# Kernel optimization log

Hardware: AMD Instinct MI355X
Metric: run time of the kernel (lower is better)

## Reference

```python
import jax, jax.numpy as jnp
import numpy as np
import math

L, B = 1024, 256
SEQ_DIM, KMER_DIM, HID = 16, 256, 64
N_LAYERS = 2
IN_DIM = SEQ_DIM + KMER_DIM + 21  # 293


def _normalize(v, eps=1e-12):
    return v / jnp.maximum(jnp.linalg.norm(v, axis=-1, keepdims=True), eps)


def _nerf_rot(a, b, c):
    # rotation matrix with columns [bc, n x bc, n] from last three backbone points
    bc = _normalize(c - b)
    n = _normalize(jnp.cross(b - a, bc))
    return jnp.stack([bc, jnp.cross(n, bc), n], axis=-1)  # (..., 3, 3)


def pnerf(c_tilde, nfrag):
    # c_tilde: (3L, B, 3) SRF coordinates; parallelized natural extension of reference frame
    Ltot, batch = c_tilde.shape[0], c_tilde.shape[1]
    k = Ltot // nfrag
    # contiguous fragments of length k, folded into the batch dim: (k, nfrag*B, 3)
    x = c_tilde.reshape(nfrag, k, batch, 3).transpose(1, 0, 2, 3).reshape(k, nfrag * batch, 3)
    init = jnp.array([[-math.sqrt(0.5), math.sqrt(1.5), 0.0],
                      [-math.sqrt(2.0), 0.0, 0.0],
                      [0.0, 0.0, 0.0]], dtype=c_tilde.dtype)
    F = nfrag * batch
    carry0 = (jnp.broadcast_to(init[0], (F, 3)),
              jnp.broadcast_to(init[1], (F, 3)),
              jnp.broadcast_to(init[2], (F, 3)))

    def extend(carry, ct):
        a, b, c = carry
        R = _nerf_rot(a, b, c)                      # (F, 3, 3)
        d = c + jnp.einsum('fij,fj->fi', R, ct)     # (F, 3)
        return (b, c, d), d

    _, frag = jax.lax.scan(extend, carry0, x)        # (k, F, 3)
    frag = frag.reshape(k, nfrag, batch, 3).transpose(1, 0, 2, 3)  # (nfrag, k, B, 3)

    # assemble fragments sequentially; init frame is identity/origin so frag 0 passes through
    carryA = (jnp.broadcast_to(init[0], (batch, 3)),
              jnp.broadcast_to(init[1], (batch, 3)),
              jnp.broadcast_to(init[2], (batch, 3)))

    def assemble(carry, fr):
        a, b, c = carry
        R = _nerf_rot(a, b, c)                      # (B, 3, 3)
        y = c + jnp.einsum('bij,kbj->kbi', R, fr)   # (k, B, 3)
        return (y[-3], y[-2], y[-1]), y

    _, ys = jax.lax.scan(assemble, carryA, frag)     # (nfrag, k, B, 3)
    return ys.reshape(nfrag * k, batch, 3)


def setup_inputs() -> dict:
    key = jax.random.key(0)
    ks = jax.random.split(key, 12)
    s = 0.05
    return {
        'seq': jax.random.randint(ks[0], (L, B), 0, 20, dtype=jnp.int64),
        'kmer': jax.random.randint(ks[1], (L, B), 0, 22 ** 3, dtype=jnp.int64),
        'pssm': jax.random.uniform(ks[2], (L, B, 21), dtype=jnp.float32),
        'length': jax.random.randint(ks[3], (L,), 1, L, dtype=jnp.int64),
        'seq_embed': jax.random.normal(ks[4], (20, SEQ_DIM), dtype=jnp.float32) * s,
        'kmer_embed': jax.random.normal(ks[5], (22 ** 3, KMER_DIM), dtype=jnp.float32) * s,
        'W0': jax.random.normal(ks[6], (IN_DIM, HID), dtype=jnp.float32) * s,
        'b0': jnp.zeros((HID,), dtype=jnp.float32),
        'We': jax.random.normal(ks[7], (HID, HID), dtype=jnp.float32) * s,
        'be': jnp.zeros((HID,), dtype=jnp.float32),
        'W1': jax.random.normal(ks[8], (HID, 9), dtype=jnp.float32) * s,
        'b1': jnp.zeros((9,), dtype=jnp.float32),
    }


def reference(seq, kmer, pssm, length, seq_embed, kmer_embed, W0, b0, We, be, W1, b1):
    s = seq_embed[seq]                                   # (L, B, 16)
    km = kmer_embed[kmer]                                # (L, B, 256)
    h = jnp.concatenate([s, km, pssm], axis=2)           # (L, B, 293)
    h = h @ W0 + b0                                      # (L, B, 64)
    # torch list-multiplication shares the SAME Linear across the n_layers blocks
    for _ in range(N_LAYERS):
        h = jax.nn.relu(h @ We + be)                     # dropout is identity at eval
    srf = h @ W1 + b1                                    # (L, B, 9)
    Ld, Bd = srf.shape[0], srf.shape[1]
    srf = srf.reshape(Ld, Bd, 3, 3).transpose(0, 2, 1, 3).reshape(3 * Ld, Bd, 3)
    return pnerf(srf, int(math.sqrt(Ld)))
```

## Files before the change

### kernel.cpp

```cpp
#include <hip/hip_runtime.h>
#include <math.h>

#define HPAD 72

typedef short bf16x8 __attribute__((ext_vector_type(8)));
typedef float f32x4  __attribute__((ext_vector_type(4)));

__device__ __forceinline__ unsigned short f2bf(float x) {
    unsigned int u = __float_as_uint(x);
    return (unsigned short)((u + 0x7FFFu + ((u >> 16) & 1u)) >> 16);
}
__device__ __forceinline__ float bf2f(unsigned short h) {
    return __uint_as_float(((unsigned int)h) << 16);
}
__device__ __forceinline__ void split2(float x, unsigned short& h, unsigned short& l) {
    h = f2bf(x);
    l = f2bf(x - bf2f(h));
}
__device__ __forceinline__ void split2t(float x, unsigned short& h, unsigned short& l) {
    unsigned int u = __float_as_uint(x);
    h = (unsigned short)(u >> 16);
    float r = x - __uint_as_float(u & 0xFFFF0000u);
    l = f2bf(r);
}

__device__ __forceinline__ float inv_norm3(float x, float y, float z) {
    float d = fmaf(x, x, fmaf(y, y, z * z));
    return rsqrtf(fmaxf(d, 1e-24f));
}
__device__ __forceinline__ float3 f3sub(float3 a, float3 b) {
    return make_float3(a.x - b.x, a.y - b.y, a.z - b.z);
}
__device__ __forceinline__ float3 f3cross(float3 a, float3 b) {
    return make_float3(a.y * b.z - a.z * b.y,
                       a.z * b.x - a.x * b.z,
                       a.x * b.y - a.y * b.x);
}
__device__ __forceinline__ void nerf_frame(const float3& A, const float3& Bv,
                                           const float3& C, float3& bc,
                                           float3& n, float3& m3) {
    float3 w  = f3sub(C, Bv);
    float3 v  = f3sub(Bv, A);
    float3 cr = f3cross(v, w);
    float iw = inv_norm3(w.x, w.y, w.z);
    float ic = inv_norm3(cr.x, cr.y, cr.z);
    bc = make_float3(w.x * iw, w.y * iw, w.z * iw);
    n  = make_float3(cr.x * ic, cr.y * ic, cr.z * ic);
    m3 = f3cross(n, bc);
}
__device__ __forceinline__ float3 nerf_place(const float3& C, const float3& bc,
                                             const float3& m3, const float3& n,
                                             float tx, float ty, float tz) {
    return make_float3(
        fmaf(m3.x, ty, fmaf(bc.x, tx, fmaf(n.x, tz, C.x))),
        fmaf(m3.y, ty, fmaf(bc.y, tx, fmaf(n.y, tz, C.y))),
        fmaf(m3.z, ty, fmaf(bc.z, tx, fmaf(n.z, tz, C.z))));
}

__global__ __launch_bounds__(256) void tables_kernel(
    const float* __restrict__ emb, const float* __restrict__ W0,
    const float* __restrict__ se, const float* __restrict__ b0,
    const float* __restrict__ We, const float* __restrict__ W1,
    float* __restrict__ kt, float* __restrict__ seqT,
    unsigned short* __restrict__ WeTH, unsigned short* __restrict__ WeTL,
    unsigned short* __restrict__ W0pTH, unsigned short* __restrict__ W0pTL,
    unsigned short* __restrict__ W1TH, unsigned short* __restrict__ W1TL) {
    int tid = threadIdx.x;
    if (blockIdx.x < 167) {
        const int lane = tid & 63;
        const int wv   = __builtin_amdgcn_readfirstlane(tid >> 6);
        const int q    = lane >> 4;
        const int c16  = lane & 15;
        const int r0   = blockIdx.x * 64;
        const int n    = wv * 16 + c16;

        bf16x8 BH[8], BL[8];
        #pragma unroll
        for (int kt8 = 0; kt8 < 8; ++kt8)
            #pragma unroll
            for (int j = 0; j < 8; ++j) {
                float w = W0[(16 + kt8 * 32 + q * 8 + j) * 64 + n];
                unsigned short h, l; split2t(w, h, l);
                BH[kt8][j] = (short)h; BL[kt8][j] = (short)l;
            }

        f32x4 acc[4];
        #pragma unroll
        for (int t = 0; t < 4; ++t) acc[t] = (f32x4){0.f, 0.f, 0.f, 0.f};

        #pragma unroll
        for (int kt8 = 0; kt8 < 8; ++kt8) {
            #pragma unroll
            for (int t = 0; t < 4; ++t) {
                int rr = r0 + t * 16 + c16;
                if (rr > 10647) rr = 10647;
                const float* ap = emb + rr * 256 + kt8 * 32 + q * 8;
                float4 a0 = *(const float4*)ap;
                float4 a1 = *(const float4*)(ap + 4);
                bf16x8 ah, al;
                unsigned short h, l;
                split2t(a0.x, h, l); ah[0] = (short)h; al[0] = (short)l;
                split2t(a0.y, h, l); ah[1] = (short)h; al[1] = (short)l;
                split2t(a0.z, h, l); ah[2] = (short)h; al[2] = (short)l;
                split2t(a0.w, h, l); ah[3] = (short)h; al[3] = (short)l;
                split2t(a1.x, h, l); ah[4] = (short)h; al[4] = (short)l;
                split2t(a1.y, h, l); ah[5] = (short)h; al[5] = (short)l;
                split2t(a1.z, h, l); ah[6] = (short)h; al[6] = (short)l;
                split2t(a1.w, h, l); ah[7] = (short)h; al[7] = (short)l;
                acc[t] = __builtin_amdgcn_mfma_f32_16x16x32_bf16(ah, BH[kt8], acc[t], 0, 0, 0);
                acc[t] = __builtin_amdgcn_mfma_f32_16x16x32_bf16(al, BH[kt8], acc[t], 0, 0, 0);
                acc[t] = __builtin_amdgcn_mfma_f32_16x16x32_bf16(ah, BL[kt8], acc[t], 0, 0, 0);
            }
        }
        #pragma unroll
        for (int t = 0; t < 4; ++t)
            #pragma unroll
            for (int r = 0; r < 4; ++r) {
                int row = r0 + t * 16 + q * 4 + r;
                if (row < 10648) kt[row * 64 + n] = acc[t][r];
            }
    } else if (blockIdx.x < 172) {
        int e = (blockIdx.x - 167) * 256 + tid;
        int r = e >> 6, j = e & 63;
        float acc = b0[j];
        #pragma unroll
        for (int k = 0; k < 16; ++k)
            acc = fmaf(se[r * 16 + k], W0[k * 64 + j], acc);
        float cs = 0.f;
        #pragma unroll
        for (int c = 0; c < 21; ++c) cs += W0[(272 + c) * 64 + j];
        seqT[r * 64 + j] = acc + 0.5f * cs;
    } else {
        #pragma unroll
        for (int i = 0; i < 16; ++i) {
            int e = i * 256 + tid;
            int k = e >> 6, n = e & 63;
            unsigned short h, l; split2(We[k * 64 + n], h, l);
            WeTH[n * 64 + k] = h; WeTL[n * 64 + k] = l;
        }
        #pragma unroll
        for (int i = 0; i < 8; ++i) {
            int e = i * 256 + tid;
            int k = e >> 6, n = e & 63;
            float w = (k < 21) ? W0[(272 + k) * 64 + n] : 0.f;
            unsigned short h, l; split2(w, h, l);
            W0pTH[n * 32 + k] = h; W0pTL[n * 32 + k] = l;
        }
        #pragma unroll
        for (int i = 0; i < 4; ++i) {
            int e = i * 256 + tid;
            int k = e >> 4, c = e & 15;
            float w = (c < 9) ? W1[k * 9 + c] : 0.f;
            unsigned short h, l; split2(w, h, l);
            W1TH[c * 64 + k] = h; W1TL[c * 64 + k] = l;
        }
    }
}

__global__ __launch_bounds__(256, 4) void mlp_kernel(
    const int* __restrict__ seq, const int* __restrict__ kmer,
    const float* __restrict__ pssm,
    const float* __restrict__ seqT, const float* __restrict__ kmerT,
    const unsigned short* __restrict__ WeTH, const unsigned short* __restrict__ WeTL,
    const unsigned short* __restrict__ W0pTH, const unsigned short* __restrict__ W0pTL,
    const unsigned short* __restrict__ W1TH, const unsigned short* __restrict__ W1TL,
    const float* __restrict__ be, const float* __restrict__ b1,
    float* __restrict__ srf_t) {

    __shared__ __align__(16) unsigned short Hah[64][HPAD];
    __shared__ __align__(16) unsigned short Hal[64][HPAD];
    __shared__ __align__(16) unsigned short Hbh[64][HPAD];
    __shared__ __align__(16) unsigned short Hbl[64][HPAD];

    const int tid  = threadIdx.x;
    const int lane = tid & 63;
    const int wv   = __builtin_amdgcn_readfirstlane(tid >> 6);
    const int q    = lane >> 4;
    const int c16  = lane & 15;
    const int m0   = blockIdx.x * 64;
    const int n    = wv * 16 + c16;

    f32x4 acc[4];
    #pragma unroll
    for (int t = 0; t < 4; ++t) {
        #pragma unroll
        for (int r = 0; r < 4; ++r) {
            int m  = t * 16 + q * 4 + r;
            int s  = seq[m0 + m];
            int km = kmer[m0 + m];
            acc[t][r] = seqT[s * 64 + n] + kmerT[km * 64 + n];
        }
    }

    bf16x8 PAH[4], PAL[4];
    #pragma unroll
    for (int t = 0; t < 4; ++t) {
        int m = m0 + t * 16 + c16;
        #pragma unroll
        for (int j = 0; j < 8; ++j) {
            int k = q * 8 + j;
            float v = (k < 21) ? (pssm[m * 21 + k] - 0.5f) : 0.f;
            unsigned short h, l; split2t(v, h, l);
            PAH[t][j] = (short)h; PAL[t][j] = (short)l;
        }
    }

    bf16x8 WeH[2], WeL[2], W1H[2], W1L[2], W0H, W0L;
    #pragma unroll
    for (int kk = 0; kk < 2; ++kk) {
        WeH[kk] = *(const bf16x8*)(WeTH + n * 64 + kk * 32 + q * 8);
        WeL[kk] = *(const bf16x8*)(WeTL + n * 64 + kk * 32 + q * 8);
        W1H[kk] = *(const bf16x8*)(W1TH + c16 * 64 + kk * 32 + q * 8);
        W1L[kk] = *(const bf16x8*)(W1TL + c16 * 64 + kk * 32 + q * 8);
    }
    W0H = *(const bf16x8*)(W0pTH + n * 32 + q * 8);
    W0L = *(const bf16x8*)(W0pTL + n * 32 + q * 8);
    const float be_n = be[n];
    const float b1h  = (c16 < 9) ? b1[c16] : 0.f;

    #pragma unroll
    for (int t = 0; t < 4; ++t) {
        acc[t] = __builtin_amdgcn_mfma_f32_16x16x32_bf16(PAH[t], W0H, acc[t], 0, 0, 0);
        acc[t] = __builtin_amdgcn_mfma_f32_16x16x32_bf16(PAL[t], W0H, acc[t], 0, 0, 0);
        acc[t] = __builtin_amdgcn_mfma_f32_16x16x32_bf16(PAH[t], W0L, acc[t], 0, 0, 0);
    }
    #pragma unroll
    for (int t = 0; t < 4; ++t)
        #pragma unroll
        for (int r = 0; r < 4; ++r) {
            unsigned short h, l; split2t(acc[t][r], h, l);
            Hah[t * 16 + q * 4 + r][n] = h;
            Hal[t * 16 + q * 4 + r][n] = l;
        }
    __syncthreads();

    {
        f32x4 a1[4];
        #pragma unroll
        for (int t = 0; t < 4; ++t) {
            a1[t] = (f32x4){be_n, be_n, be_n, be_n};
            #pragma unroll
            for (int kk = 0; kk < 2; ++kk) {
                bf16x8 ah = *(const bf16x8*)&Hah[t * 16 + c16][kk * 32 + q * 8];
                bf16x8 al = *(const bf16x8*)&Hal[t * 16 + c16][kk * 32 + q * 8];
                a1[t] = __builtin_amdgcn_mfma_f32_16x16x32_bf16(ah, WeH[kk], a1[t], 0, 0, 0);
                a1[t] = __builtin_amdgcn_mfma_f32_16x16x32_bf16(al, WeH[kk], a1[t], 0, 0, 0);
                a1[t] = __builtin_amdgcn_mfma_f32_16x16x32_bf16(ah, WeL[kk], a1[t], 0, 0, 0);
            }
        }
        #pragma unroll
        for (int t = 0; t < 4; ++t)
            #pragma unroll
            for (int r = 0; r < 4; ++r) {
                unsigned short h, l; split2t(fmaxf(a1[t][r], 0.f), h, l);
                Hbh[t * 16 + q * 4 + r][n] = h;
                Hbl[t * 16 + q * 4 + r][n] = l;
            }
        __syncthreads();
    }
    {
        f32x4 a2[4];
        #pragma unroll
        for (int t = 0; t < 4; ++t) {
            a2[t] = (f32x4){be_n, be_n, be_n, be_n};
            #pragma unroll
            for (int kk = 0; kk < 2; ++kk) {
                bf16x8 ah = *(const bf16x8*)&Hbh[t * 16 + c16][kk * 32 + q * 8];
                bf16x8 al = *(const bf16x8*)&Hbl[t * 16 + c16][kk * 32 + q * 8];
                a2[t] = __builtin_amdgcn_mfma_f32_16x16x32_bf16(ah, WeH[kk], a2[t], 0, 0, 0);
                a2[t] = __builtin_amdgcn_mfma_f32_16x16x32_bf16(al, WeH[kk], a2[t], 0, 0, 0);
                a2[t] = __builtin_amdgcn_mfma_f32_16x16x32_bf16(ah, WeL[kk], a2[t], 0, 0, 0);
            }
        }
        #pragma unroll
        for (int t = 0; t < 4; ++t)
            #pragma unroll
            for (int r = 0; r < 4; ++r) {
                unsigned short h, l; split2t(fmaxf(a2[t][r], 0.f), h, l);
                Hah[t * 16 + q * 4 + r][n] = h;
                Hal[t * 16 + q * 4 + r][n] = l;
            }
        __syncthreads();
    }

    {
        f32x4 ah4 = (f32x4){b1h, b1h, b1h, b1h};
        #pragma unroll
        for (int kk = 0; kk < 2; ++kk) {
            bf16x8 ah = *(const bf16x8*)&Hah[wv * 16 + c16][kk * 32 + q * 8];
            bf16x8 al = *(const bf16x8*)&Hal[wv * 16 + c16][kk * 32 + q * 8];
            ah4 = __builtin_amdgcn_mfma_f32_16x16x32_bf16(ah, W1H[kk], ah4, 0, 0, 0);
            ah4 = __builtin_amdgcn_mfma_f32_16x16x32_bf16(al, W1H[kk], ah4, 0, 0, 0);
            ah4 = __builtin_amdgcn_mfma_f32_16x16x32_bf16(ah, W1L[kk], ah4, 0, 0, 0);
        }
        if (c16 < 9) {
            #pragma unroll
            for (int r = 0; r < 4; ++r) {
                int pos = m0 + wv * 16 + q * 4 + r;
                int l = pos >> 8, b = pos & 255;
                srf_t[(l * 9 + c16) * 256 + b] = ah4[r];
            }
        }
    }
}

__global__ __launch_bounds__(64) void extend_kernel(
    const float* __restrict__ srf_t, float* __restrict__ fragbuf,
    float* __restrict__ FPbuf) {
    int frag = blockIdx.x >> 2;
    int bb   = ((blockIdx.x & 3) << 6) + threadIdx.x;

    float3 A  = make_float3(-0.70710678118654752f, 1.22474487139158905f, 0.f);
    float3 Bv = make_float3(-1.41421356237309505f, 0.f, 0.f);
    float3 C  = make_float3(0.f, 0.f, 0.f);

    float ct0[9], ct1[9], ct2[9], ct3[9];
    #pragma unroll
    for (int m = 0; m < 9; ++m) {
        ct0[m] = srf_t[((frag * 32 + 0) * 9 + m) * 256 + bb];
        ct1[m] = srf_t[((frag * 32 + 1) * 9 + m) * 256 + bb];
        ct2[m] = srf_t[((frag * 32 + 2) * 9 + m) * 256 + bb];
    }

    for (int ll = 0; ll < 32; ++ll) {
        if (ll < 29) {
            #pragma unroll
            for (int m = 0; m < 9; ++m)
                ct3[m] = srf_t[((frag * 32 + ll + 3) * 9 + m) * 256 + bb];
        } else {
            #pragma unroll
            for (int m = 0; m < 9; ++m) ct3[m] = 0.f;
        }
        #pragma unroll
        for (int s3 = 0; s3 < 3; ++s3) {
            float3 bc, nn, m3;
            nerf_frame(A, Bv, C, bc, nn, m3);
            float3 d = nerf_place(C, bc, m3, nn,
                                  ct0[3 * s3 + 0], ct0[3 * s3 + 1], ct0[3 * s3 + 2]);
            int row = frag * 96 + ll * 3 + s3;
            fragbuf[(row * 3 + 0) * 256 + bb] = d.x;
            fragbuf[(row * 3 + 1) * 256 + bb] = d.y;
            fragbuf[(row * 3 + 2) * 256 + bb] = d.z;
            A = Bv; Bv = C; C = d;
        }
        #pragma unroll
        for (int m = 0; m < 9; ++m) { ct0[m] = ct1[m]; ct1[m] = ct2[m]; ct2[m] = ct3[m]; }
    }

    float3 bc, nn, m3;
    nerf_frame(A, Bv, C, bc, nn, m3);
    FPbuf[(frag * 12 + 0)  * 256 + bb] = bc.x;
    FPbuf[(frag * 12 + 1)  * 256 + bb] = bc.y;
    FPbuf[(frag * 12 + 2)  * 256 + bb] = bc.z;
    FPbuf[(frag * 12 + 3)  * 256 + bb] = m3.x;
    FPbuf[(frag * 12 + 4)  * 256 + bb] = m3.y;
    FPbuf[(frag * 12 + 5)  * 256 + bb] = m3.z;
    FPbuf[(frag * 12 + 6)  * 256 + bb] = nn.x;
    FPbuf[(frag * 12 + 7)  * 256 + bb] = nn.y;
    FPbuf[(frag * 12 + 8)  * 256 + bb] = nn.z;
    FPbuf[(frag * 12 + 9)  * 256 + bb] = C.x;
    FPbuf[(frag * 12 + 10) * 256 + bb] = C.y;
    FPbuf[(frag * 12 + 11) * 256 + bb] = C.z;
}

__global__ __launch_bounds__(256) void carry_kernel(
    const float* __restrict__ FPbuf, float4* __restrict__ frames) {
    __shared__ float S[384][64];
    int tid  = threadIdx.x;
    int base = blockIdx.x * 64;
    for (int i = tid; i < 384 * 64; i += 256) {
        int row = i >> 6, col = i & 63;
        S[row][col] = FPbuf[row * 256 + base + col];
    }
    __syncthreads();
    if (tid < 64) {
        int bb = base + tid;
        float3 ob = make_float3(1.f, 0.f, 0.f);
        float3 om = make_float3(0.f, 1.f, 0.f);
        float3 on = make_float3(0.f, 0.f, 1.f);
        float3 c  = make_float3(0.f, 0.f, 0.f);
        for (int f = 0; f < 32; ++f) {
            int fb = (f * 256 + bb) * 3;
            frames[fb + 0] = make_float4(ob.x, ob.y, ob.z, om.x);
            frames[fb + 1] = make_float4(om.y, om.z, on.x, on.y);
            frames[fb + 2] = make_float4(on.z, c.x, c.y, c.z);

            int r0 = f * 12;
            float3 Fb = make_float3(S[r0+0][tid], S[r0+1][tid], S[r0+2][tid]);
            float3 Fm = make_float3(S[r0+3][tid], S[r0+4][tid], S[r0+5][tid]);
            float3 Fn = make_float3(S[r0+6][tid], S[r0+7][tid], S[r0+8][tid]);
            float3 p  = make_float3(S[r0+9][tid], S[r0+10][tid], S[r0+11][tid]);

            float3 nb = make_float3(
                fmaf(ob.x,Fb.x, fmaf(om.x,Fb.y, on.x*Fb.z)),
                fmaf(ob.y,Fb.x, fmaf(om.y,Fb.y, on.y*Fb.z)),
                fmaf(ob.z,Fb.x, fmaf(om.z,Fb.y, on.z*Fb.z)));
            float3 nm = make_float3(
                fmaf(ob.x,Fm.x, fmaf(om.x,Fm.y, on.x*Fm.z)),
                fmaf(ob.y,Fm.x, fmaf(om.y,Fm.y, on.y*Fm.z)),
                fmaf(ob.z,Fm.x, fmaf(om.z,Fm.y, on.z*Fm.z)));
            float3 nn = make_float3(
                fmaf(ob.x,Fn.x, fmaf(om.x,Fn.y, on.x*Fn.z)),
                fmaf(ob.y,Fn.x, fmaf(om.y,Fn.y, on.y*Fn.z)),
                fmaf(ob.z,Fn.x, fmaf(om.z,Fn.y, on.z*Fn.z)));
            float3 nc = make_float3(
                fmaf(ob.x,p.x, fmaf(om.x,p.y, fmaf(on.x,p.z, c.x))),
                fmaf(ob.y,p.x, fmaf(om.y,p.y, fmaf(on.y,p.z, c.y))),
                fmaf(ob.z,p.x, fmaf(om.z,p.y, fmaf(on.z,p.z, c.z))));
            ob = nb; om = nm; on = nn; c = nc;
        }
    }
}

__global__ __launch_bounds__(256) void apply_kernel(
    const float* __restrict__ fragbuf, const float4* __restrict__ frames,
    float* __restrict__ out) {
    __shared__ float sm[768];
    int bb   = threadIdx.x;
    int row  = blockIdx.x;
    int frag = row / 96;

    float fx = fragbuf[(row * 3 + 0) * 256 + bb];
    float fy = fragbuf[(row * 3 + 1) * 256 + bb];
    float fz = fragbuf[(row * 3 + 2) * 256 + bb];

    int fb = (frag * 256 + bb) * 3;
    float4 f0 = frames[fb + 0];
    float4 f1 = frames[fb + 1];
    float4 f2 = frames[fb + 2];

    sm[bb * 3 + 0] = f2.y + f0.x * fx + f0.w * fy + f1.z * fz;
    sm[bb * 3 + 1] = f2.z + f0.y * fx + f1.x * fy + f1.w * fz;
    sm[bb * 3 + 2] = f2.w + f0.z * fx + f1.y * fy + f2.x * fz;
    __syncthreads();

    int base = row * 768;
    out[base + bb]       = sm[bb];
    out[base + 256 + bb] = sm[256 + bb];
    out[base + 512 + bb] = sm[512 + bb];
}

extern "C" void kernel_launch(void* const* d_in, const int* in_sizes, int n_in,
                              void* d_out, int out_size, void* d_ws, size_t ws_size,
                              hipStream_t stream) {
    const int*   seq        = (const int*)d_in[0];
    const int*   kmer       = (const int*)d_in[1];
    const float* pssm       = (const float*)d_in[2];
    const float* seq_embed  = (const float*)d_in[4];
    const float* kmer_embed = (const float*)d_in[5];
    const float* W0         = (const float*)d_in[6];
    const float* b0         = (const float*)d_in[7];
    const float* We         = (const float*)d_in[8];
    const float* be         = (const float*)d_in[9];
    const float* W1         = (const float*)d_in[10];
    const float* b1         = (const float*)d_in[11];

    float* ws      = (float*)d_ws;
    float* kmerT   = ws;
    float* seqT    = kmerT + 681472;
    float* srf_t   = seqT + 1280;
    float* fragbuf = srf_t + 2359296;
    float* frames  = fragbuf + 2359296;
    float* FPbuf   = frames + 98304;
    float* out     = (float*)d_out;

    unsigned short* WeTH  = (unsigned short*)fragbuf;
    unsigned short* WeTL  = WeTH + 4096;
    unsigned short* W0pTH = WeTL + 4096;
    unsigned short* W0pTL = W0pTH + 2048;
    unsigned short* W1TH  = W0pTL + 2048;
    unsigned short* W1TL  = W1TH + 1024;

    hipLaunchKernelGGL(tables_kernel, dim3(173), dim3(256), 0, stream,
                       kmer_embed, W0, seq_embed, b0, We, W1,
                       kmerT, seqT, WeTH, WeTL, W0pTH, W0pTL, W1TH, W1TL);
    hipLaunchKernelGGL(mlp_kernel, dim3(4096), dim3(256), 0, stream,
                       seq, kmer, pssm, seqT, kmerT,
                       WeTH, WeTL, W0pTH, W0pTL, W1TH, W1TL,
                       be, b1, srf_t);
    hipLaunchKernelGGL(extend_kernel, dim3(128), dim3(64), 0, stream,
                       srf_t, fragbuf, FPbuf);
    hipLaunchKernelGGL(carry_kernel, dim3(4), dim3(256), 0, stream,
                       FPbuf, (float4*)frames);
    hipLaunchKernelGGL(apply_kernel, dim3(3072), dim3(256), 0, stream,
                       fragbuf, (float4*)frames, out);
}
```

Before: 196.9 us.

## Keep MLP activations in registers via transposed MFMA and bpermute, dropping LDS

The MLP kernel now computes the transposed product, with weights as the A operand and activations as the B operand. Each wave owns 16 rows end to end, so hidden activations pass between layers through ds_bpermute shuffles instead of shared-memory round trips and block barriers. Each wave now holds all 64 output columns of We in registers, which raises register pressure. The occupancy hint in launch_bounds is dropped, and the final output store pattern changes.

```diff
diff --git a/kernel.cpp b/kernel.cpp
--- a/kernel.cpp
+++ b/kernel.cpp
@@ -1,7 +1,5 @@
 #include <hip/hip_runtime.h>
 #include <math.h>
-
-#define HPAD 72
 
 typedef short bf16x8 __attribute__((ext_vector_type(8)));
 typedef float f32x4  __attribute__((ext_vector_type(4)));
@@ -22,6 +20,11 @@
     h = (unsigned short)(u >> 16);
     float r = x - __uint_as_float(u & 0xFFFF0000u);
     l = f2bf(r);
+}
+
+__device__ __forceinline__ float bperm(int src_lane, float v) {
+    return __int_as_float(
+        __builtin_amdgcn_ds_bpermute(src_lane << 2, __float_as_int(v)));
 }
 
 __device__ __forceinline__ float inv_norm3(float x, float y, float z) {
@@ -157,7 +160,7 @@
     }
 }
 
-__global__ __launch_bounds__(256, 4) void mlp_kernel(
+__global__ __launch_bounds__(256) void mlp_kernel(
     const int* __restrict__ seq, const int* __restrict__ kmer,
     const float* __restrict__ pssm,
     const float* __restrict__ seqT, const float* __restrict__ kmerT,
@@ -167,139 +170,121 @@
     const float* __restrict__ be, const float* __restrict__ b1,
     float* __restrict__ srf_t) {
 
-    __shared__ __align__(16) unsigned short Hah[64][HPAD];
-    __shared__ __align__(16) unsigned short Hal[64][HPAD];
-    __shared__ __align__(16) unsigned short Hbh[64][HPAD];
-    __shared__ __align__(16) unsigned short Hbl[64][HPAD];
-
     const int tid  = threadIdx.x;
     const int lane = tid & 63;
-    const int wv   = __builtin_amdgcn_readfirstlane(tid >> 6);
-    const int q    = lane >> 4;
-    const int c16  = lane & 15;
-    const int m0   = blockIdx.x * 64;
-    const int n    = wv * 16 + c16;
-
+    const int wv   = tid >> 6;
+    const int qb   = lane >> 4;
+    const int m    = lane & 15;
+    const int c16  = m;
+    const int p    = blockIdx.x * 64 + wv * 16 + m;
+    const int srcbase = ((qb & 1) << 5) + m;
+
+    const int s  = seq[p];
+    const int km = kmer[p];
     f32x4 acc[4];
     #pragma unroll
     for (int t = 0; t < 4; ++t) {
+        float4 sv = *(const float4*)(seqT + s * 64 + 16 * t + 4 * qb);
+        float4 kv = *(const float4*)(kmerT + km * 64 + 16 * t + 4 * qb);
+        acc[t] = (f32x4){sv.x + kv.x, sv.y + kv.y, sv.z + kv.z, sv.w + kv.w};
+    }
+
+    bf16x8 PBH, PBL;
+    #pragma unroll
+    for (int jj = 0; jj < 8; ++jj) {
+        int k = qb * 8 + jj;
+        float v = (k < 21) ? (pssm[p * 21 + k] - 0.5f) : 0.f;
+        unsigned short h, l; split2t(v, h, l);
+        PBH[jj] = (short)h; PBL[jj] = (short)l;
+    }
+
+    #pragma unroll
+    for (int t = 0; t < 4; ++t) {
+        bf16x8 AH = *(const bf16x8*)(W0pTH + (16 * t + c16) * 32 + qb * 8);
+        bf16x8 AL = *(const bf16x8*)(W0pTL + (16 * t + c16) * 32 + qb * 8);
+        acc[t] = __builtin_amdgcn_mfma_f32_16x16x32_bf16(AH, PBH, acc[t], 0, 0, 0);
+        acc[t] = __builtin_amdgcn_mfma_f32_16x16x32_bf16(AL, PBH, acc[t], 0, 0, 0);
+        acc[t] = __builtin_amdgcn_mfma_f32_16x16x32_bf16(AH, PBL, acc[t], 0, 0, 0);
+    }
+
+    bf16x8 WeH[4][2], WeL[4][2];
+    #pragma unroll
+    for (int t = 0; t < 4; ++t)
+        #pragma unroll
+        for (int kk = 0; kk < 2; ++kk) {
+            WeH[t][kk] = *(const bf16x8*)(WeTH + (16 * t + c16) * 64 + kk * 32 + qb * 8);
+            WeL[t][kk] = *(const bf16x8*)(WeTL + (16 * t + c16) * 64 + kk * 32 + qb * 8);
+        }
+    float4 beq[4];
+    #pragma unroll
+    for (int t = 0; t < 4; ++t)
+        beq[t] = *(const float4*)(be + 16 * t + 4 * qb);
+
+    #pragma unroll
+    for (int layer = 0; layer < 2; ++layer) {
+        bf16x8 GBH[2], GBL[2];
+        #pragma unroll
+        for (int kk = 0; kk < 2; ++kk) {
+            #pragma unroll
+            for (int jj = 0; jj < 8; ++jj) {
+                int r   = jj & 3;
+                int off = (jj >> 2) << 4;
+                float va = bperm(srcbase + off, acc[2 * kk][r]);
+                float vb = bperm(srcbase + off, acc[2 * kk + 1][r]);
+                float g  = (lane & 32) ? vb : va;
+                unsigned short h, l; split2t(g, h, l);
+                GBH[kk][jj] = (short)h; GBL[kk][jj] = (short)l;
+            }
+        }
+        #pragma unroll
+        for (int t = 0; t < 4; ++t) {
+            f32x4 a = (f32x4){beq[t].x, beq[t].y, beq[t].z, beq[t].w};
+            #pragma unroll
+            for (int kk = 0; kk < 2; ++kk) {
+                a = __builtin_amdgcn_mfma_f32_16x16x32_bf16(WeH[t][kk], GBH[kk], a, 0, 0, 0);
+                a = __builtin_amdgcn_mfma_f32_16x16x32_bf16(WeL[t][kk], GBH[kk], a, 0, 0, 0);
+                a = __builtin_amdgcn_mfma_f32_16x16x32_bf16(WeH[t][kk], GBL[kk], a, 0, 0, 0);
+            }
+            acc[t] = (f32x4){fmaxf(a[0], 0.f), fmaxf(a[1], 0.f),
+                             fmaxf(a[2], 0.f), fmaxf(a[3], 0.f)};
+        }
+    }
+
+    {
+        bf16x8 GBH[2], GBL[2];
+        #pragma unroll
+        for (int kk = 0; kk < 2; ++kk) {
+            #pragma unroll
+            for (int jj = 0; jj < 8; ++jj) {
+                int r   = jj & 3;
+                int off = (jj >> 2) << 4;
+                float va = bperm(srcbase + off, acc[2 * kk][r]);
+                float vb = bperm(srcbase + off, acc[2 * kk + 1][r]);
+                float g  = (lane & 32) ? vb : va;
+                unsigned short h, l; split2t(g, h, l);
+                GBH[kk][jj] = (short)h; GBL[kk][jj] = (short)l;
+            }
+        }
+        f32x4 a;
         #pragma unroll
         for (int r = 0; r < 4; ++r) {
-            int m  = t * 16 + q * 4 + r;
-            int s  = seq[m0 + m];
-            int km = kmer[m0 + m];
-            acc[t][r] = seqT[s * 64 + n] + kmerT[km * 64 + n];
-        }
-    }
-
-    bf16x8 PAH[4], PAL[4];
-    #pragma unroll
-    for (int t = 0; t < 4; ++t) {
-        int m = m0 + t * 16 + c16;
-        #pragma unroll
-        for (int j = 0; j < 8; ++j) {
-            int k = q * 8 + j;
-            float v = (k < 21) ? (pssm[m * 21 + k] - 0.5f) : 0.f;
-            unsigned short h, l; split2t(v, h, l);
-            PAH[t][j] = (short)h; PAL[t][j] = (short)l;
-        }
-    }
-
-    bf16x8 WeH[2], WeL[2], W1H[2], W1L[2], W0H, W0L;
-    #pragma unroll
-    for (int kk = 0; kk < 2; ++kk) {
-        WeH[kk] = *(const bf16x8*)(WeTH + n * 64 + kk * 32 + q * 8);
-        WeL[kk] = *(const bf16x8*)(WeTL + n * 64 + kk * 32 + q * 8);
-        W1H[kk] = *(const bf16x8*)(W1TH + c16 * 64 + kk * 32 + q * 8);
-        W1L[kk] = *(const bf16x8*)(W1TL + c16 * 64 + kk * 32 + q * 8);
-    }
-    W0H = *(const bf16x8*)(W0pTH + n * 32 + q * 8);
-    W0L = *(const bf16x8*)(W0pTL + n * 32 + q * 8);
-    const float be_n = be[n];
-    const float b1h  = (c16 < 9) ? b1[c16] : 0.f;
-
-    #pragma unroll
-    for (int t = 0; t < 4; ++t) {
-        acc[t] = __builtin_amdgcn_mfma_f32_16x16x32_bf16(PAH[t], W0H, acc[t], 0, 0, 0);
-        acc[t] = __builtin_amdgcn_mfma_f32_16x16x32_bf16(PAL[t], W0H, acc[t], 0, 0, 0);
-        acc[t] = __builtin_amdgcn_mfma_f32_16x16x32_bf16(PAH[t], W0L, acc[t], 0, 0, 0);
-    }
-    #pragma unroll
-    for (int t = 0; t < 4; ++t)
+            int c = 4 * qb + r;
+            a[r] = (c < 9) ? b1[c] : 0.f;
+        }
+        #pragma unroll
+        for (int kk = 0; kk < 2; ++kk) {
+            bf16x8 AH = *(const bf16x8*)(W1TH + c16 * 64 + kk * 32 + qb * 8);
+            bf16x8 AL = *(const bf16x8*)(W1TL + c16 * 64 + kk * 32 + qb * 8);
+            a = __builtin_amdgcn_mfma_f32_16x16x32_bf16(AH, GBH[kk], a, 0, 0, 0);
+            a = __builtin_amdgcn_mfma_f32_16x16x32_bf16(AL, GBH[kk], a, 0, 0, 0);
+            a = __builtin_amdgcn_mfma_f32_16x16x32_bf16(AH, GBL[kk], a, 0, 0, 0);
+        }
+        const int l = p >> 8, b = p & 255;
         #pragma unroll
         for (int r = 0; r < 4; ++r) {
-            unsigned short h, l; split2t(acc[t][r], h, l);
-            Hah[t * 16 + q * 4 + r][n] = h;
-            Hal[t * 16 + q * 4 + r][n] = l;
-        }
-    __syncthreads();
-
-    {
-        f32x4 a1[4];
-        #pragma unroll
-        for (int t = 0; t < 4; ++t) {
-            a1[t] = (f32x4){be_n, be_n, be_n, be_n};
-            #pragma unroll
-            for (int kk = 0; kk < 2; ++kk) {
-                bf16x8 ah = *(const bf16x8*)&Hah[t * 16 + c16][kk * 32 + q * 8];
-                bf16x8 al = *(const bf16x8*)&Hal[t * 16 + c16][kk * 32 + q * 8];
-                a1[t] = __builtin_amdgcn_mfma_f32_16x16x32_bf16(ah, WeH[kk], a1[t], 0, 0, 0);
-                a1[t] = __builtin_amdgcn_mfma_f32_16x16x32_bf16(al, WeH[kk], a1[t], 0, 0, 0);
-                a1[t] = __builtin_amdgcn_mfma_f32_16x16x32_bf16(ah, WeL[kk], a1[t], 0, 0, 0);
-            }
-        }
-        #pragma unroll
-        for (int t = 0; t < 4; ++t)
-            #pragma unroll
-            for (int r = 0; r < 4; ++r) {
-                unsigned short h, l; split2t(fmaxf(a1[t][r], 0.f), h, l);
-                Hbh[t * 16 + q * 4 + r][n] = h;
-                Hbl[t * 16 + q * 4 + r][n] = l;
-            }
-        __syncthreads();
-    }
-    {
-        f32x4 a2[4];
-        #pragma unroll
-        for (int t = 0; t < 4; ++t) {
-            a2[t] = (f32x4){be_n, be_n, be_n, be_n};
-            #pragma unroll
-            for (int kk = 0; kk < 2; ++kk) {
-                bf16x8 ah = *(const bf16x8*)&Hbh[t * 16 + c16][kk * 32 + q * 8];
-                bf16x8 al = *(const bf16x8*)&Hbl[t * 16 + c16][kk * 32 + q * 8];
-                a2[t] = __builtin_amdgcn_mfma_f32_16x16x32_bf16(ah, WeH[kk], a2[t], 0, 0, 0);
-                a2[t] = __builtin_amdgcn_mfma_f32_16x16x32_bf16(al, WeH[kk], a2[t], 0, 0, 0);
-                a2[t] = __builtin_amdgcn_mfma_f32_16x16x32_bf16(ah, WeL[kk], a2[t], 0, 0, 0);
-            }
-        }
-        #pragma unroll
-        for (int t = 0; t < 4; ++t)
-            #pragma unroll
-            for (int r = 0; r < 4; ++r) {
-                unsigned short h, l; split2t(fmaxf(a2[t][r], 0.f), h, l);
-                Hah[t * 16 + q * 4 + r][n] = h;
-                Hal[t * 16 + q * 4 + r][n] = l;
-            }
-        __syncthreads();
-    }
-
-    {
-        f32x4 ah4 = (f32x4){b1h, b1h, b1h, b1h};
-        #pragma unroll
-        for (int kk = 0; kk < 2; ++kk) {
-            bf16x8 ah = *(const bf16x8*)&Hah[wv * 16 + c16][kk * 32 + q * 8];
-            bf16x8 al = *(const bf16x8*)&Hal[wv * 16 + c16][kk * 32 + q * 8];
-            ah4 = __builtin_amdgcn_mfma_f32_16x16x32_bf16(ah, W1H[kk], ah4, 0, 0, 0);
-            ah4 = __builtin_amdgcn_mfma_f32_16x16x32_bf16(al, W1H[kk], ah4, 0, 0, 0);
-            ah4 = __builtin_amdgcn_mfma_f32_16x16x32_bf16(ah, W1L[kk], ah4, 0, 0, 0);
-        }
-        if (c16 < 9) {
-            #pragma unroll
-            for (int r = 0; r < 4; ++r) {
-                int pos = m0 + wv * 16 + q * 4 + r;
-                int l = pos >> 8, b = pos & 255;
-                srf_t[(l * 9 + c16) * 256 + b] = ah4[r];
-            }
+            int c = 4 * qb + r;
+            if (c < 9)
+                srf_t[(l * 9 + c) * 256 + b] = a[r];
         }
     }
 }
```

New measurement: 206.0 us. 4.6% more time.

## Fuse pipeline into persistent cooperative megakernel with grid syncs

Applied to the files above, without the earlier changes.

Replaces the five kernel launches with one cooperative persistent kernel that runs each phase in grid-strided loops separated by grid.sync(), keeping the old launches as a fallback. It also stages seq/kmer indices and the pssm tile (bf16 hi/lo split) in shared memory inside the MLP phase, and splits the carry phase over 16 blocks instead of 4. The aim is to remove launch gaps and tail effects between dependent stages. The cost is grid-wide barrier overhead, fewer blocks than a normal launch for the large phases, and more register/LDS pressure from sharing one kernel across all phases.

```diff
diff --git a/kernel.cpp b/kernel.cpp
--- a/kernel.cpp
+++ b/kernel.cpp
@@ -1,7 +1,8 @@
 #include <hip/hip_runtime.h>
+#include <hip/hip_cooperative_groups.h>
 #include <math.h>
 
-#define HPAD 72
+namespace cg = cooperative_groups;
 
 typedef short bf16x8 __attribute__((ext_vector_type(8)));
 typedef float f32x4  __attribute__((ext_vector_type(4)));
@@ -57,21 +58,23 @@
         fmaf(m3.z, ty, fmaf(bc.z, tx, fmaf(n.z, tz, C.z))));
 }
 
-__global__ __launch_bounds__(256) void tables_kernel(
-    const float* __restrict__ emb, const float* __restrict__ W0,
-    const float* __restrict__ se, const float* __restrict__ b0,
-    const float* __restrict__ We, const float* __restrict__ W1,
-    float* __restrict__ kt, float* __restrict__ seqT,
-    unsigned short* __restrict__ WeTH, unsigned short* __restrict__ WeTL,
-    unsigned short* __restrict__ W0pTH, unsigned short* __restrict__ W0pTL,
-    unsigned short* __restrict__ W1TH, unsigned short* __restrict__ W1TL) {
-    int tid = threadIdx.x;
-    if (blockIdx.x < 167) {
+struct KParams {
+    const int* seq; const int* kmer; const float* pssm;
+    const float* se; const float* emb;
+    const float* W0; const float* b0; const float* We; const float* be;
+    const float* W1; const float* b1;
+    float* kmerT; float* seqT; float* srf_t; float* fragbuf;
+    float4* frames; float* FPbuf; float* out;
+    unsigned short *WeTH, *WeTL, *W0pTH, *W0pTL, *W1TH, *W1TL;
+};
+
+__device__ __forceinline__ void phase_tables(int vb, int tid, const KParams& P) {
+    if (vb < 167) {
         const int lane = tid & 63;
         const int wv   = __builtin_amdgcn_readfirstlane(tid >> 6);
         const int q    = lane >> 4;
         const int c16  = lane & 15;
-        const int r0   = blockIdx.x * 64;
+        const int r0   = vb * 64;
         const int n    = wv * 16 + c16;
 
         bf16x8 BH[8], BL[8];
@@ -79,22 +82,20 @@
         for (int kt8 = 0; kt8 < 8; ++kt8)
             #pragma unroll
             for (int j = 0; j < 8; ++j) {
-                float w = W0[(16 + kt8 * 32 + q * 8 + j) * 64 + n];
+                float w = P.W0[(16 + kt8 * 32 + q * 8 + j) * 64 + n];
                 unsigned short h, l; split2t(w, h, l);
                 BH[kt8][j] = (short)h; BL[kt8][j] = (short)l;
             }
-
         f32x4 acc[4];
         #pragma unroll
         for (int t = 0; t < 4; ++t) acc[t] = (f32x4){0.f, 0.f, 0.f, 0.f};
-
         #pragma unroll
         for (int kt8 = 0; kt8 < 8; ++kt8) {
             #pragma unroll
             for (int t = 0; t < 4; ++t) {
                 int rr = r0 + t * 16 + c16;
                 if (rr > 10647) rr = 10647;
-                const float* ap = emb + rr * 256 + kt8 * 32 + q * 8;
+                const float* ap = P.emb + rr * 256 + kt8 * 32 + q * 8;
                 float4 a0 = *(const float4*)ap;
                 float4 a1 = *(const float4*)(ap + 4);
                 bf16x8 ah, al;
@@ -117,112 +118,110 @@
             #pragma unroll
             for (int r = 0; r < 4; ++r) {
                 int row = r0 + t * 16 + q * 4 + r;
-                if (row < 10648) kt[row * 64 + n] = acc[t][r];
-            }
-    } else if (blockIdx.x < 172) {
-        int e = (blockIdx.x - 167) * 256 + tid;
+                if (row < 10648) P.kmerT[row * 64 + n] = acc[t][r];
+            }
+    } else if (vb < 172) {
+        int e = (vb - 167) * 256 + tid;
         int r = e >> 6, j = e & 63;
-        float acc = b0[j];
+        float acc = P.b0[j];
         #pragma unroll
         for (int k = 0; k < 16; ++k)
-            acc = fmaf(se[r * 16 + k], W0[k * 64 + j], acc);
+            acc = fmaf(P.se[r * 16 + k], P.W0[k * 64 + j], acc);
         float cs = 0.f;
         #pragma unroll
-        for (int c = 0; c < 21; ++c) cs += W0[(272 + c) * 64 + j];
-        seqT[r * 64 + j] = acc + 0.5f * cs;
+        for (int c = 0; c < 21; ++c) cs += P.W0[(272 + c) * 64 + j];
+        P.seqT[r * 64 + j] = acc + 0.5f * cs;
     } else {
         #pragma unroll
         for (int i = 0; i < 16; ++i) {
             int e = i * 256 + tid;
             int k = e >> 6, n = e & 63;
-            unsigned short h, l; split2(We[k * 64 + n], h, l);
-            WeTH[n * 64 + k] = h; WeTL[n * 64 + k] = l;
+            unsigned short h, l; split2(P.We[k * 64 + n], h, l);
+            P.WeTH[n * 64 + k] = h; P.WeTL[n * 64 + k] = l;
         }
         #pragma unroll
         for (int i = 0; i < 8; ++i) {
             int e = i * 256 + tid;
             int k = e >> 6, n = e & 63;
-            float w = (k < 21) ? W0[(272 + k) * 64 + n] : 0.f;
+            float w = (k < 21) ? P.W0[(272 + k) * 64 + n] : 0.f;
             unsigned short h, l; split2(w, h, l);
-            W0pTH[n * 32 + k] = h; W0pTL[n * 32 + k] = l;
+            P.W0pTH[n * 32 + k] = h; P.W0pTL[n * 32 + k] = l;
         }
         #pragma unroll
         for (int i = 0; i < 4; ++i) {
             int e = i * 256 + tid;
             int k = e >> 4, c = e & 15;
-            float w = (c < 9) ? W1[k * 9 + c] : 0.f;
+            float w = (c < 9) ? P.W1[k * 9 + c] : 0.f;
             unsigned short h, l; split2(w, h, l);
-            W1TH[c * 64 + k] = h; W1TL[c * 64 + k] = l;
-        }
-    }
-}
-
-__global__ __launch_bounds__(256, 4) void mlp_kernel(
-    const int* __restrict__ seq, const int* __restrict__ kmer,
-    const float* __restrict__ pssm,
-    const float* __restrict__ seqT, const float* __restrict__ kmerT,
-    const unsigned short* __restrict__ WeTH, const unsigned short* __restrict__ WeTL,
-    const unsigned short* __restrict__ W0pTH, const unsigned short* __restrict__ W0pTL,
-    const unsigned short* __restrict__ W1TH, const unsigned short* __restrict__ W1TL,
-    const float* __restrict__ be, const float* __restrict__ b1,
-    float* __restrict__ srf_t) {
-
-    __shared__ __align__(16) unsigned short Hah[64][HPAD];
-    __shared__ __align__(16) unsigned short Hal[64][HPAD];
-    __shared__ __align__(16) unsigned short Hbh[64][HPAD];
-    __shared__ __align__(16) unsigned short Hbl[64][HPAD];
-
-    const int tid  = threadIdx.x;
+            P.W1TH[c * 64 + k] = h; P.W1TL[c * 64 + k] = l;
+        }
+    }
+}
+
+__device__ __forceinline__ void phase_mlp(int m0, int tid, unsigned char* SMEM,
+                                          const KParams& P) {
+    unsigned short (*Hah)[72] = (unsigned short (*)[72])(SMEM);
+    unsigned short (*Hal)[72] = (unsigned short (*)[72])(SMEM + 9216);
+    unsigned short (*Hbh)[72] = (unsigned short (*)[72])(SMEM + 18432);
+    unsigned short (*Hbl)[72] = (unsigned short (*)[72])(SMEM + 27648);
+    unsigned short (*Ph)[40]  = (unsigned short (*)[40])(SMEM + 18432);
+    unsigned short (*Pl)[40]  = (unsigned short (*)[40])(SMEM + 18432 + 5120);
+    int* sidx = (int*)(SMEM + 36864);
+    int* kidx = sidx + 64;
+
     const int lane = tid & 63;
     const int wv   = __builtin_amdgcn_readfirstlane(tid >> 6);
     const int q    = lane >> 4;
     const int c16  = lane & 15;
-    const int m0   = blockIdx.x * 64;
     const int n    = wv * 16 + c16;
+
+    __syncthreads();
+
+    if (tid < 64) {
+        sidx[tid] = P.seq[m0 + tid];
+        kidx[tid] = P.kmer[m0 + tid];
+    }
+    for (int i = tid; i < 64 * 21; i += 256) {
+        float v = P.pssm[m0 * 21 + i] - 0.5f;
+        unsigned short h, l; split2t(v, h, l);
+        Ph[i / 21][i % 21] = h;
+        Pl[i / 21][i % 21] = l;
+    }
+    for (int i = tid; i < 64 * 11; i += 256) {
+        Ph[i / 11][21 + (i % 11)] = 0;
+        Pl[i / 11][21 + (i % 11)] = 0;
+    }
+
+    bf16x8 WeH[2], WeL[2], W1H[2], W1L[2], W0H, W0L;
+    #pragma unroll
+    for (int kk = 0; kk < 2; ++kk) {
+        WeH[kk] = *(const bf16x8*)(P.WeTH + n * 64 + kk * 32 + q * 8);
+        WeL[kk] = *(const bf16x8*)(P.WeTL + n * 64 + kk * 32 + q * 8);
+        W1H[kk] = *(const bf16x8*)(P.W1TH + c16 * 64 + kk * 32 + q * 8);
+        W1L[kk] = *(const bf16x8*)(P.W1TL + c16 * 64 + kk * 32 + q * 8);
+    }
+    W0H = *(const bf16x8*)(P.W0pTH + n * 32 + q * 8);
+    W0L = *(const bf16x8*)(P.W0pTL + n * 32 + q * 8);
+    const float be_n = P.be[n];
+    const float b1h  = (c16 < 9) ? P.b1[c16] : 0.f;
+    __syncthreads();
 
     f32x4 acc[4];
     #pragma unroll
     for (int t = 0; t < 4; ++t) {
         #pragma unroll
         for (int r = 0; r < 4; ++r) {
-            int m  = t * 16 + q * 4 + r;
-            int s  = seq[m0 + m];
-            int km = kmer[m0 + m];
-            acc[t][r] = seqT[s * 64 + n] + kmerT[km * 64 + n];
-        }
-    }
-
-    bf16x8 PAH[4], PAL[4];
+            int m = t * 16 + q * 4 + r;
+            acc[t][r] = P.seqT[sidx[m] * 64 + n] + P.kmerT[kidx[m] * 64 + n];
+        }
+    }
     #pragma unroll
     for (int t = 0; t < 4; ++t) {
-        int m = m0 + t * 16 + c16;
-        #pragma unroll
-        for (int j = 0; j < 8; ++j) {
-            int k = q * 8 + j;
-            float v = (k < 21) ? (pssm[m * 21 + k] - 0.5f) : 0.f;
-            unsigned short h, l; split2t(v, h, l);
-            PAH[t][j] = (short)h; PAL[t][j] = (short)l;
-        }
-    }
-
-    bf16x8 WeH[2], WeL[2], W1H[2], W1L[2], W0H, W0L;
-    #pragma unroll
-    for (int kk = 0; kk < 2; ++kk) {
-        WeH[kk] = *(const bf16x8*)(WeTH + n * 64 + kk * 32 + q * 8);
-        WeL[kk] = *(const bf16x8*)(WeTL + n * 64 + kk * 32 + q * 8);
-        W1H[kk] = *(const bf16x8*)(W1TH + c16 * 64 + kk * 32 + q * 8);
-        W1L[kk] = *(const bf16x8*)(W1TL + c16 * 64 + kk * 32 + q * 8);
-    }
-    W0H = *(const bf16x8*)(W0pTH + n * 32 + q * 8);
-    W0L = *(const bf16x8*)(W0pTL + n * 32 + q * 8);
-    const float be_n = be[n];
-    const float b1h  = (c16 < 9) ? b1[c16] : 0.f;
-
-    #pragma unroll
-    for (int t = 0; t < 4; ++t) {
-        acc[t] = __builtin_amdgcn_mfma_f32_16x16x32_bf16(PAH[t], W0H, acc[t], 0, 0, 0);
-        acc[t] = __builtin_amdgcn_mfma_f32_16x16x32_bf16(PAL[t], W0H, acc[t], 0, 0, 0);
-        acc[t] = __builtin_amdgcn_mfma_f32_16x16x32_bf16(PAH[t], W0L, acc[t], 0, 0, 0);
+        bf16x8 ah = *(const bf16x8*)&Ph[t * 16 + c16][q * 8];
+        bf16x8 al = *(const bf16x8*)&Pl[t * 16 + c16][q * 8];
+        acc[t] = __builtin_amdgcn_mfma_f32_16x16x32_bf16(ah, W0H, acc[t], 0, 0, 0);
+        acc[t] = __builtin_amdgcn_mfma_f32_16x16x32_bf16(al, W0H, acc[t], 0, 0, 0);
+        acc[t] = __builtin_amdgcn_mfma_f32_16x16x32_bf16(ah, W0L, acc[t], 0, 0, 0);
     }
     #pragma unroll
     for (int t = 0; t < 4; ++t)
@@ -282,7 +281,6 @@
             }
         __syncthreads();
     }
-
     {
         f32x4 ah4 = (f32x4){b1h, b1h, b1h, b1h};
         #pragma unroll
@@ -298,17 +296,16 @@
             for (int r = 0; r < 4; ++r) {
                 int pos = m0 + wv * 16 + q * 4 + r;
                 int l = pos >> 8, b = pos & 255;
-                srf_t[(l * 9 + c16) * 256 + b] = ah4[r];
-            }
-        }
-    }
-}
-
-__global__ __launch_bounds__(64) void extend_kernel(
-    const float* __restrict__ srf_t, float* __restrict__ fragbuf,
-    float* __restrict__ FPbuf) {
-    int frag = blockIdx.x >> 2;
-    int bb   = ((blockIdx.x & 3) << 6) + threadIdx.x;
+                P.srf_t[(l * 9 + c16) * 256 + b] = ah4[r];
+            }
+        }
+    }
+}
+
+__device__ __forceinline__ void phase_extend(int vb, int tid, const KParams& P) {
+    if (tid >= 64) return;
+    int frag = vb >> 2;
+    int bb   = ((vb & 3) << 6) + tid;
 
     float3 A  = make_float3(-0.70710678118654752f, 1.22474487139158905f, 0.f);
     float3 Bv = make_float3(-1.41421356237309505f, 0.f, 0.f);
@@ -317,16 +314,15 @@
     float ct0[9], ct1[9], ct2[9], ct3[9];
     #pragma unroll
     for (int m = 0; m < 9; ++m) {
-        ct0[m] = srf_t[((frag * 32 + 0) * 9 + m) * 256 + bb];
-        ct1[m] = srf_t[((frag * 32 + 1) * 9 + m) * 256 + bb];
-        ct2[m] = srf_t[((frag * 32 + 2) * 9 + m) * 256 + bb];
-    }
-
+        ct0[m] = P.srf_t[((frag * 32 + 0) * 9 + m) * 256 + bb];
+        ct1[m] = P.srf_t[((frag * 32 + 1) * 9 + m) * 256 + bb];
+        ct2[m] = P.srf_t[((frag * 32 + 2) * 9 + m) * 256 + bb];
+    }
     for (int ll = 0; ll < 32; ++ll) {
         if (ll < 29) {
             #pragma unroll
             for (int m = 0; m < 9; ++m)
-                ct3[m] = srf_t[((frag * 32 + ll + 3) * 9 + m) * 256 + bb];
+                ct3[m] = P.srf_t[((frag * 32 + ll + 3) * 9 + m) * 256 + bb];
         } else {
             #pragma unroll
             for (int m = 0; m < 9; ++m) ct3[m] = 0.f;
@@ -338,42 +334,39 @@
             float3 d = nerf_place(C, bc, m3, nn,
                                   ct0[3 * s3 + 0], ct0[3 * s3 + 1], ct0[3 * s3 + 2]);
             int row = frag * 96 + ll * 3 + s3;
-            fragbuf[(row * 3 + 0) * 256 + bb] = d.x;
-            fragbuf[(row * 3 + 1) * 256 + bb] = d.y;
-            fragbuf[(row * 3 + 2) * 256 + bb] = d.z;
+            P.fragbuf[(row * 3 + 0) * 256 + bb] = d.x;
+            P.fragbuf[(row * 3 + 1) * 256 + bb] = d.y;
+            P.fragbuf[(row * 3 + 2) * 256 + bb] = d.z;
             A = Bv; Bv = C; C = d;
         }
         #pragma unroll
         for (int m = 0; m < 9; ++m) { ct0[m] = ct1[m]; ct1[m] = ct2[m]; ct2[m] = ct3[m]; }
     }
-
     float3 bc, nn, m3;
     nerf_frame(A, Bv, C, bc, nn, m3);
-    FPbuf[(frag * 12 + 0)  * 256 + bb] = bc.x;
-    FPbuf[(frag * 12 + 1)  * 256 + bb] = bc.y;
-    FPbuf[(frag * 12 + 2)  * 256 + bb] = bc.z;
-    FPbuf[(frag * 12 + 3)  * 256 + bb] = m3.x;
-    FPbuf[(frag * 12 + 4)  * 256 + bb] = m3.y;
-    FPbuf[(frag * 12 + 5)  * 256 + bb] = m3.z;
-    FPbuf[(frag * 12 + 6)  * 256 + bb] = nn.x;
-    FPbuf[(frag * 12 + 7)  * 256 + bb] = nn.y;
-    FPbuf[(frag * 12 + 8)  * 256 + bb] = nn.z;
-    FPbuf[(frag * 12 + 9)  * 256 + bb] = C.x;
-    FPbuf[(frag * 12 + 10) * 256 + bb] = C.y;
-    FPbuf[(frag * 12 + 11) * 256 + bb] = C.z;
-}
-
-__global__ __launch_bounds__(256) void carry_kernel(
-    const float* __restrict__ FPbuf, float4* __restrict__ frames) {
-    __shared__ float S[384][64];
-    int tid  = threadIdx.x;
-    int base = blockIdx.x * 64;
-    for (int i = tid; i < 384 * 64; i += 256) {
-        int row = i >> 6, col = i & 63;
-        S[row][col] = FPbuf[row * 256 + base + col];
+    P.FPbuf[(frag * 12 + 0)  * 256 + bb] = bc.x;
+    P.FPbuf[(frag * 12 + 1)  * 256 + bb] = bc.y;
+    P.FPbuf[(frag * 12 + 2)  * 256 + bb] = bc.z;
+    P.FPbuf[(frag * 12 + 3)  * 256 + bb] = m3.x;
+    P.FPbuf[(frag * 12 + 4)  * 256 + bb] = m3.y;
+    P.FPbuf[(frag * 12 + 5)  * 256 + bb] = m3.z;
+    P.FPbuf[(frag * 12 + 6)  * 256 + bb] = nn.x;
+    P.FPbuf[(frag * 12 + 7)  * 256 + bb] = nn.y;
+    P.FPbuf[(frag * 12 + 8)  * 256 + bb] = nn.z;
+    P.FPbuf[(frag * 12 + 9)  * 256 + bb] = C.x;
+    P.FPbuf[(frag * 12 + 10) * 256 + bb] = C.y;
+    P.FPbuf[(frag * 12 + 11) * 256 + bb] = C.z;
+}
+
+__device__ __forceinline__ void phase_carry(int vb, int tid, float (*S)[16],
+                                            const KParams& P) {
+    int base = vb * 16;
+    for (int i = tid; i < 384 * 16; i += 256) {
+        int row = i >> 4, col = i & 15;
+        S[row][col] = P.FPbuf[row * 256 + base + col];
     }
     __syncthreads();
-    if (tid < 64) {
+    if (tid < 16) {
         int bb = base + tid;
         float3 ob = make_float3(1.f, 0.f, 0.f);
         float3 om = make_float3(0.f, 1.f, 0.f);
@@ -381,9 +374,9 @@
         float3 c  = make_float3(0.f, 0.f, 0.f);
         for (int f = 0; f < 32; ++f) {
             int fb = (f * 256 + bb) * 3;
-            frames[fb + 0] = make_float4(ob.x, ob.y, ob.z, om.x);
-            frames[fb + 1] = make_float4(om.y, om.z, on.x, on.y);
-            frames[fb + 2] = make_float4(on.z, c.x, c.y, c.z);
+            P.frames[fb + 0] = make_float4(ob.x, ob.y, ob.z, om.x);
+            P.frames[fb + 1] = make_float4(om.y, om.z, on.x, on.y);
+            P.frames[fb + 2] = make_float4(on.z, c.x, c.y, c.z);
 
             int r0 = f * 12;
             float3 Fb = make_float3(S[r0+0][tid], S[r0+1][tid], S[r0+2][tid]);
@@ -399,7 +392,7 @@
                 fmaf(ob.x,Fm.x, fmaf(om.x,Fm.y, on.x*Fm.z)),
                 fmaf(ob.y,Fm.x, fmaf(om.y,Fm.y, on.y*Fm.z)),
                 fmaf(ob.z,Fm.x, fmaf(om.z,Fm.y, on.z*Fm.z)));
-            float3 nn = make_float3(
+            float3 nn2 = make_float3(
                 fmaf(ob.x,Fn.x, fmaf(om.x,Fn.y, on.x*Fn.z)),
                 fmaf(ob.y,Fn.x, fmaf(om.y,Fn.y, on.y*Fn.z)),
                 fmaf(ob.z,Fn.x, fmaf(om.z,Fn.y, on.z*Fn.z)));
@@ -407,54 +400,81 @@
                 fmaf(ob.x,p.x, fmaf(om.x,p.y, fmaf(on.x,p.z, c.x))),
                 fmaf(ob.y,p.x, fmaf(om.y,p.y, fmaf(on.y,p.z, c.y))),
                 fmaf(ob.z,p.x, fmaf(om.z,p.y, fmaf(on.z,p.z, c.z))));
-            ob = nb; om = nm; on = nn; c = nc;
-        }
-    }
-}
-
-__global__ __launch_bounds__(256) void apply_kernel(
-    const float* __restrict__ fragbuf, const float4* __restrict__ frames,
-    float* __restrict__ out) {
-    __shared__ float sm[768];
-    int bb   = threadIdx.x;
-    int row  = blockIdx.x;
+            ob = nb; om = nm; on = nn2; c = nc;
+        }
+    }
+}
+
+__device__ __forceinline__ void phase_apply(int row, int tid, float* sm,
+                                            const KParams& P) {
     int frag = row / 96;
-
-    float fx = fragbuf[(row * 3 + 0) * 256 + bb];
-    float fy = fragbuf[(row * 3 + 1) * 256 + bb];
-    float fz = fragbuf[(row * 3 + 2) * 256 + bb];
+    int bb   = tid;
+
+    float fx = P.fragbuf[(row * 3 + 0) * 256 + bb];
+    float fy = P.fragbuf[(row * 3 + 1) * 256 + bb];
+    float fz = P.fragbuf[(row * 3 + 2) * 256 + bb];
 
     int fb = (frag * 256 + bb) * 3;
-    float4 f0 = frames[fb + 0];
-    float4 f1 = frames[fb + 1];
-    float4 f2 = frames[fb + 2];
-
+    float4 f0 = P.frames[fb + 0];
+    float4 f1 = P.frames[fb + 1];
+    float4 f2 = P.frames[fb + 2];
+
+    __syncthreads();
     sm[bb * 3 + 0] = f2.y + f0.x * fx + f0.w * fy + f1.z * fz;
     sm[bb * 3 + 1] = f2.z + f0.y * fx + f1.x * fy + f1.w * fz;
     sm[bb * 3 + 2] = f2.w + f0.z * fx + f1.y * fy + f2.x * fz;
     __syncthreads();
 
     int base = row * 768;
-    out[base + bb]       = sm[bb];
-    out[base + 256 + bb] = sm[256 + bb];
-    out[base + 512 + bb] = sm[512 + bb];
+    P.out[base + bb]       = sm[bb];
+    P.out[base + 256 + bb] = sm[256 + bb];
+    P.out[base + 512 + bb] = sm[512 + bb];
+}
+
+__global__ __launch_bounds__(256) void tables_kernel(KParams P) {
+    phase_tables(blockIdx.x, threadIdx.x, P);
+}
+__global__ __launch_bounds__(256, 4) void mlp_kernel(KParams P) {
+    __shared__ __align__(16) unsigned char SMEM[37376];
+    phase_mlp(blockIdx.x * 64, threadIdx.x, SMEM, P);
+}
+__global__ __launch_bounds__(64) void extend_kernel(KParams P) {
+    phase_extend(blockIdx.x, threadIdx.x, P);
+}
+__global__ __launch_bounds__(256) void carry_kernel(KParams P) {
+    __shared__ float S[384][16];
+    phase_carry(blockIdx.x, threadIdx.x, S, P);
+}
+__global__ __launch_bounds__(256) void apply_kernel(KParams P) {
+    __shared__ float sm[768];
+    phase_apply(blockIdx.x, threadIdx.x, sm, P);
+}
+
+__global__ __launch_bounds__(256, 4) void mega_kernel(KParams P) {
+    cg::grid_group grid = cg::this_grid();
+    __shared__ __align__(16) unsigned char SMEM[37376];
+    const int tid = threadIdx.x;
+    const int GD  = gridDim.x;
+
+    for (int vb = blockIdx.x; vb < 173; vb += GD)
+        phase_tables(vb, tid, P);
+    grid.sync();
+    for (int vb = blockIdx.x; vb < 4096; vb += GD)
+        phase_mlp(vb * 64, tid, SMEM, P);
+    grid.sync();
+    for (int vb = blockIdx.x; vb < 128; vb += GD)
+        phase_extend(vb, tid, P);
+    grid.sync();
+    for (int vb = blockIdx.x; vb < 16; vb += GD)
+        phase_carry(vb, tid, (float (*)[16])SMEM, P);
+    grid.sync();
+    for (int vb = blockIdx.x; vb < 3072; vb += GD)
+        phase_apply(vb, tid, (float*)SMEM, P);
 }
 
 extern "C" void kernel_launch(void* const* d_in, const int* in_sizes, int n_in,
                               void* d_out, int out_size, void* d_ws, size_t ws_size,
                               hipStream_t stream) {
-    const int*   seq        = (const int*)d_in[0];
-    const int*   kmer       = (const int*)d_in[1];
-    const float* pssm       = (const float*)d_in[2];
-    const float* seq_embed  = (const float*)d_in[4];
-    const float* kmer_embed = (const float*)d_in[5];
-    const float* W0         = (const float*)d_in[6];
-    const float* b0         = (const float*)d_in[7];
-    const float* We         = (const float*)d_in[8];
-    const float* be         = (const float*)d_in[9];
-    const float* W1         = (const float*)d_in[10];
-    const float* b1         = (const float*)d_in[11];
-
     float* ws      = (float*)d_ws;
     float* kmerT   = ws;
     float* seqT    = kmerT + 681472;
@@ -462,7 +482,6 @@
     float* fragbuf = srf_t + 2359296;
     float* frames  = fragbuf + 2359296;
     float* FPbuf   = frames + 98304;
-    float* out     = (float*)d_out;
 
     unsigned short* WeTH  = (unsigned short*)fragbuf;
     unsigned short* WeTL  = WeTH + 4096;
@@ -471,17 +490,41 @@
     unsigned short* W1TH  = W0pTL + 2048;
     unsigned short* W1TL  = W1TH + 1024;
 
-    hipLaunchKernelGGL(tables_kernel, dim3(173), dim3(256), 0, stream,
-                       kmer_embed, W0, seq_embed, b0, We, W1,
-                       kmerT, seqT, WeTH, WeTL, W0pTH, W0pTL, W1TH, W1TL);
-    hipLaunchKernelGGL(mlp_kernel, dim3(4096), dim3(256), 0, stream,
-                       seq, kmer, pssm, seqT, kmerT,
-                       WeTH, WeTL, W0pTH, W0pTL, W1TH, W1TL,
-                       be, b1, srf_t);
-    hipLaunchKernelGGL(extend_kernel, dim3(128), dim3(64), 0, stream,
-                       srf_t, fragbuf, FPbuf);
-    hipLaunchKernelGGL(carry_kernel, dim3(4), dim3(256), 0, stream,
-                       FPbuf, (float4*)frames);
-    hipLaunchKernelGGL(apply_kernel, dim3(3072), dim3(256), 0, stream,
-                       fragbuf, (float4*)frames, out);
-}
+    KParams P;
+    P.seq  = (const int*)d_in[0];
+    P.kmer = (const int*)d_in[1];
+    P.pssm = (const float*)d_in[2];
+    P.se   = (const float*)d_in[4];
+    P.emb  = (const float*)d_in[5];
+    P.W0   = (const float*)d_in[6];
+    P.b0   = (const float*)d_in[7];
+    P.We   = (const float*)d_in[8];
+    P.be   = (const float*)d_in[9];
+    P.W1   = (const float*)d_in[10];
+    P.b1   = (const float*)d_in[11];
+    P.kmerT = kmerT; P.seqT = seqT; P.srf_t = srf_t; P.fragbuf = fragbuf;
+    P.frames = (float4*)frames; P.FPbuf = FPbuf; P.out = (float*)d_out;
+    P.WeTH = WeTH; P.WeTL = WeTL; P.W0pTH = W0pTH; P.W0pTL = W0pTL;
+    P.W1TH = W1TH; P.W1TL = W1TL;
+
+    bool coop_done = false;
+    int nb = 0;
+    hipError_t qe = hipOccupancyMaxActiveBlocksPerMultiprocessor(
+        &nb, reinterpret_cast<const void*>(&mega_kernel), 256, 0);
+    if (qe == hipSuccess && nb > 0) {
+        int grid = nb * 256;
+        if (grid > 1024) grid = 1024;
+        void* args[] = { (void*)&P };
+        hipError_t le = hipLaunchCooperativeKernel(
+            reinterpret_cast<const void*>(&mega_kernel), dim3(grid), dim3(256),
+            args, 0, stream);
+        coop_done = (le == hipSuccess);
+    }
+    if (!coop_done) {
+        hipLaunchKernelGGL(tables_kernel, dim3(173),  dim3(256), 0, stream, P);
+        hipLaunchKernelGGL(mlp_kernel,    dim3(4096), dim3(256), 0, stream, P);
+        hipLaunchKernelGGL(extend_kernel, dim3(128),  dim3(64),  0, stream, P);
+        hipLaunchKernelGGL(carry_kernel,  dim3(16),   dim3(256), 0, stream, P);
+        hipLaunchKernelGGL(apply_kernel,  dim3(3072), dim3(256), 0, stream, P);
+    }
+}
```

Measured after the change: 466.5 us. 137% more time.
